# Kernel tuning notes

Measured on AMD Instinct MI355X. Metric: run time of the kernel, lower is better.

## Reference

```python
import jax, jax.numpy as jnp
import numpy as np

B, T, D, H = 8, 2048, 1024, 128  # batch, seq, input_size, head_size


def setup_inputs() -> dict:
    key = jax.random.key(0)
    kx, kq, kk, kv = jax.random.split(key, 4)
    s = 1.0 / np.sqrt(D)
    return {
        "x": jax.random.normal(kx, (B, T, D), dtype=jnp.float32),
        "Wq": jax.random.normal(kq, (D, H), dtype=jnp.float32) * s,
        "Wk": jax.random.normal(kk, (D, H), dtype=jnp.float32) * s,
        "Wv": jax.random.normal(kv, (D, H), dtype=jnp.float32) * s,
    }


def reference(x, Wq, Wk, Wv):
    # projections (Linear, no bias)
    q = jnp.einsum("btd,dh->bth", x, Wq)
    k = jnp.einsum("btd,dh->bth", x, Wk)
    v = jnp.einsum("btd,dh->bth", x, Wv)
    scale = H ** (-0.5)
    scores = jnp.einsum("bth,bsh->bts", q, k) * scale  # [B,T,T]
    t = x.shape[1]
    causal = jnp.tril(jnp.ones((t, t), dtype=bool))
    scores = jnp.where(causal, scores, -jnp.inf)
    attn = jax.nn.softmax(scores, axis=-1)  # dropout p=0.0 -> identity
    out = jnp.einsum("bts,bsh->bth", attn, v)
    return out
```

## Files before the change

### kernel.cpp

```cpp
#include <hip/hip_runtime.h>
#include <math.h>

#define B_ 8
#define T_ 2048
#define D_ 1024
#define H_ 128
#define BT (B_ * T_)

typedef short bf16x8 __attribute__((ext_vector_type(8)));
typedef short bf16x4 __attribute__((ext_vector_type(4)));
typedef float f32x4 __attribute__((ext_vector_type(4)));
typedef int i32x2 __attribute__((ext_vector_type(2)));

static constexpr float SCALE = 0.08838834764831845f;

__device__ inline unsigned short f2b(float f) {
  unsigned int u = __float_as_uint(f);
  u += 0x7FFF + ((u >> 16) & 1);
  return (unsigned short)(u >> 16);
}
__device__ inline unsigned int pk2(float a, float b) {
  return (unsigned int)f2b(a) | ((unsigned int)f2b(b) << 16);
}
__device__ __forceinline__ unsigned int pk2f(float a, float b) {
  unsigned int r;
  asm("v_cvt_pk_bf16_f32 %0, %1, %2" : "=v"(r) : "v"(a), "v"(b));
  return r;
}
__device__ __forceinline__ void mfma16(f32x4& d, bf16x4 a, bf16x4 b) {
  asm("v_mfma_f32_16x16x16_bf16 %0, %1, %2, %0" : "+v"(d) : "v"(a), "v"(b));
}

__device__ __forceinline__ void gll16(const void* g, void* l) {
  __builtin_amdgcn_global_load_lds(
      (const __attribute__((address_space(1))) void*)g,
      (__attribute__((address_space(3))) void*)l, 16, 0, 0);
}

__global__ __launch_bounds__(256) void wcvt_kernel(
    const float* __restrict__ Wq, const float* __restrict__ Wk,
    const float* __restrict__ Wv, short* __restrict__ Wt) {
  __shared__ short Wls[128 * 72];
  const int sel = blockIdx.y;
  const float* W = sel == 0 ? Wq : (sel == 1 ? Wk : Wv);
  const int d0 = blockIdx.x * 64;
  const int tid = threadIdx.x;
#pragma unroll
  for (int i = 0; i < 8; ++i) {
    int slot = tid + i * 256;
    int r = slot >> 5, hg = slot & 31;
    float4 w = *(const float4*)(W + (size_t)(d0 + r) * H_ + hg * 4);
    Wls[(hg * 4 + 0) * 72 + r] = (short)f2b(w.x);
    Wls[(hg * 4 + 1) * 72 + r] = (short)f2b(w.y);
    Wls[(hg * 4 + 2) * 72 + r] = (short)f2b(w.z);
    Wls[(hg * 4 + 3) * 72 + r] = (short)f2b(w.w);
  }
  __syncthreads();
  short* dst = Wt + (size_t)sel * D_ * H_;
#pragma unroll
  for (int i = 0; i < 4; ++i) {
    int slot = tid + i * 256;
    int h = slot >> 3, g = slot & 7;
    *(int4*)(dst + (size_t)h * D_ + d0 + g * 8) = *(int4*)&Wls[h * 72 + g * 8];
  }
}

__global__ __launch_bounds__(256) void proj_kernel(
    const float* __restrict__ x, const short* __restrict__ Wt,
    short* __restrict__ qb, short* __restrict__ kb, short* __restrict__ vtb) {
  __shared__ alignas(16) char smem[49152];
  short* Xs0 = (short*)smem;
  short* Xs1 = (short*)(smem + 8192);
  short* Ws0 = (short*)(smem + 16384);
  short* Ws1 = (short*)(smem + 32768);

  const int tid = threadIdx.x;
  const int wave = tid >> 6, lane = tid & 63;
  const int ln = lane & 15, quad = lane >> 4;
  const int mw = wave & 1, nw = wave >> 1;
  const int sel = blockIdx.y;
  const int row0 = blockIdx.x * 64;
  const short* W = Wt + (size_t)sel * (size_t)(D_ * H_);

  f32x4 acc[2][4];
#pragma unroll
  for (int mi = 0; mi < 2; ++mi)
#pragma unroll
    for (int ni = 0; ni < 4; ++ni) acc[mi][ni] = (f32x4){0.f, 0.f, 0.f, 0.f};

  auto stage = [&](int bf, int k0) {
    short* Ws = bf ? Ws1 : Ws0;
#pragma unroll
    for (int j = 0; j < 4; ++j) {
      const int rbase = wave * 32 + j * 8;
      const int n = rbase + (lane >> 3);
      const int gp = (lane & 7) ^ (n & 7);
      gll16(W + (size_t)n * D_ + k0 + gp * 8, (char*)Ws + rbase * 128);
    }
    short* Xs = bf ? Xs1 : Xs0;
    float4 xr[4];
#pragma unroll
    for (int i = 0; i < 4; ++i) {
      int fid = tid + i * 256;
      int r = fid >> 4, g4 = fid & 15;
      xr[i] = *(const float4*)(x + (size_t)(row0 + r) * D_ + k0 + g4 * 4);
    }
#pragma unroll
    for (int i = 0; i < 4; ++i) {
      int fid = tid + i * 256;
      int r = fid >> 4, g4 = fid & 15;
      int g = g4 >> 1, half = g4 & 1;
      unsigned int* p = (unsigned int*)&Xs[r * 64 + ((g ^ (r & 7)) * 8) + half * 4];
      p[0] = pk2f(xr[i].x, xr[i].y);
      p[1] = pk2f(xr[i].z, xr[i].w);
    }
  };

  stage(0, 0);
  for (int s = 0; s < 16; ++s) {
    __syncthreads();
    if (s < 15) stage((s + 1) & 1, (s + 1) * 64);
    const short* Xs = (s & 1) ? Xs1 : Xs0;
    const short* Ws = (s & 1) ? Ws1 : Ws0;
#pragma unroll
    for (int kk = 0; kk < 2; ++kk) {
      bf16x8 a[2];
#pragma unroll
      for (int mi = 0; mi < 2; ++mi) {
        int r = mw * 32 + mi * 16 + ln;
        a[mi] = *(bf16x8*)&Xs[r * 64 + (((kk * 4 + quad) ^ (r & 7)) * 8)];
      }
#pragma unroll
      for (int ni = 0; ni < 4; ++ni) {
        int n = nw * 64 + ni * 16 + ln;
        bf16x8 bb = *(bf16x8*)&Ws[n * 64 + (((kk * 4 + quad) ^ (n & 7)) * 8)];
#pragma unroll
        for (int mi = 0; mi < 2; ++mi)
          acc[mi][ni] = __builtin_amdgcn_mfma_f32_16x16x32_bf16(a[mi], bb, acc[mi][ni], 0, 0, 0);
      }
    }
  }

  __syncthreads();
  short* Cs = (short*)smem;
  if (sel < 2) {
    short* out = sel ? kb : qb;
#pragma unroll
    for (int mi = 0; mi < 2; ++mi)
#pragma unroll
      for (int ni = 0; ni < 4; ++ni)
#pragma unroll
        for (int rr = 0; rr < 4; ++rr)
          Cs[(mw * 32 + mi * 16 + quad * 4 + rr) * 136 + nw * 64 + ni * 16 + ln] =
              (short)f2b(acc[mi][ni][rr]);
    __syncthreads();
#pragma unroll
    for (int i = 0; i < 4; ++i) {
      int slot = tid + i * 256;
      int r = slot >> 4, g = slot & 15;
      *(int4*)(out + (size_t)(row0 + r) * H_ + g * 8) = *(int4*)&Cs[r * 136 + g * 8];
    }
  } else {
#pragma unroll
    for (int mi = 0; mi < 2; ++mi)
#pragma unroll
      for (int ni = 0; ni < 4; ++ni)
#pragma unroll
        for (int rr = 0; rr < 4; ++rr)
          Cs[(nw * 64 + ni * 16 + ln) * 72 + mw * 32 + mi * 16 + quad * 4 + rr] =
              (short)f2b(acc[mi][ni][rr]);
    __syncthreads();
    const int b = row0 >> 11, t0 = row0 & 2047;
#pragma unroll
    for (int i = 0; i < 4; ++i) {
      int slot = tid + i * 256;
      int h = slot >> 3, g = slot & 7;
      *(int4*)(vtb + (size_t)(b * H_ + h) * T_ + t0 + g * 8) = *(int4*)&Cs[h * 72 + g * 8];
    }
  }
}

__global__ __launch_bounds__(256, 5) void attn_part(
    const short* __restrict__ qb, const short* __restrict__ kb,
    const short* __restrict__ vtb, float* __restrict__ po,
    float* __restrict__ pm, float* __restrict__ pl,
    float* __restrict__ out) {
  __shared__ alignas(16) char smem[32768];
  short* Ks0 = (short*)smem;
  short* Ks1 = (short*)(smem + 8192);
  short* Vt0 = (short*)(smem + 16384);
  short* Vt1 = (short*)(smem + 24576);

  const int tid = threadIdx.x;
  const int wv = tid >> 6, lane = tid & 63;
  const int ln = lane & 15, quad = lane >> 4;
  const int b = blockIdx.x & 7;
  const int rr = 79 - (blockIdx.x >> 3);
  const int g = (rr >= 48) ? 3 : (rr >= 24) ? 2 : (rr >= 8) ? 1 : 0;
  const int local = rr - 4 * g * (g + 1);
  const int j = 8 * g + local / (g + 1);
  const int s = local - (local / (g + 1)) * (g + 1);
  const int nseg = g + 1;
  const int sid = b * 80 + rr;
  const int q0 = j * 64;
  const int nchunks = min(16, 2 * (j + 1) - 16 * s);

  const int qglob = q0 + wv * 16 + ln;

  bf16x8 qfr[4];
#pragma unroll
  for (int kk = 0; kk < 4; ++kk)
    qfr[kk] = *(const bf16x8*)(qb + (size_t)(b * T_ + q0 + wv * 16 + ln) * H_ +
                               kk * 32 + quad * 8);

  f32x4 oacc[8];
#pragma unroll
  for (int ht = 0; ht < 8; ++ht) oacc[ht] = (f32x4){0.f, 0.f, 0.f, 0.f};

  float m_run = -INFINITY, l_run = 0.f;

  auto stageK = [&](short* dst, int s0) {
#pragma unroll
    for (int jj = 0; jj < 2; ++jj) {
      const int rb = wv * 8 + jj * 4;
      const int r = rb + (lane >> 4);
      const int gp = (lane & 15) ^ (r & 7);
      gll16(kb + (size_t)(b * T_ + s0 + r) * H_ + gp * 8, (char*)dst + rb * 256);
    }
  };
  auto stageV = [&](short* dst, int s0) {
#pragma unroll
    for (int jj = 0; jj < 2; ++jj) {
      const int hb = wv * 32 + jj * 16;
      const int h = hb + (lane >> 2);
      const int gp = (lane & 3) ^ (h & 3) ^ ((h >> 2) & 3);
      gll16(vtb + (size_t)(b * H_ + h) * T_ + s0 + gp * 8, (char*)dst + hb * 64);
    }
  };

  stageK(Ks0, 512 * s);
  stageV(Vt0, 512 * s);

  for (int ch = 0; ch < nchunks; ++ch) {
    const int s0 = 512 * s + ch * 32;
    const int cur = ch & 1;
    __syncthreads();
    if (ch + 1 < nchunks) {
      stageK(cur ? Ks0 : Ks1, s0 + 32);
      stageV(cur ? Vt0 : Vt1, s0 + 32);
    }
    const short* Kc = cur ? Ks1 : Ks0;
    const short* Vc = cur ? Vt1 : Vt0;

    f32x4 sacc[2];
#pragma unroll
    for (int t = 0; t < 2; ++t) sacc[t] = (f32x4){0.f, 0.f, 0.f, 0.f};
#pragma unroll
    for (int kk = 0; kk < 4; ++kk) {
#pragma unroll
      for (int t = 0; t < 2; ++t) {
        const int krow = t * 16 + ln;
        bf16x8 kf = *(bf16x8*)&Kc[krow * 128 + (((kk * 4 + quad) ^ (krow & 7)) * 8)];
        sacc[t] = __builtin_amdgcn_mfma_f32_16x16x32_bf16(kf, qfr[kk], sacc[t], 0, 0, 0);
      }
    }

    float sv[2][4];
    float mc = -INFINITY;
    if (s0 + 31 <= q0 + wv * 16) {
#pragma unroll
      for (int t = 0; t < 2; ++t)
#pragma unroll
        for (int r = 0; r < 4; ++r) {
          sv[t][r] = sacc[t][r] * SCALE;
          mc = fmaxf(mc, sv[t][r]);
        }
    } else {
#pragma unroll
      for (int t = 0; t < 2; ++t)
#pragma unroll
        for (int r = 0; r < 4; ++r) {
          const int key = s0 + t * 16 + quad * 4 + r;
          float sc = sacc[t][r] * SCALE;
          sv[t][r] = (key <= qglob) ? sc : -INFINITY;
          mc = fmaxf(mc, sv[t][r]);
        }
    }
    mc = fmaxf(mc, __shfl_xor(mc, 16));
    mc = fmaxf(mc, __shfl_xor(mc, 32));

    if (!__all(mc <= m_run + 8.f)) {
      const float mnew = fmaxf(m_run, mc);
      const float alpha = __expf(m_run - mnew);
#pragma unroll
      for (int ht = 0; ht < 8; ++ht)
#pragma unroll
        for (int r = 0; r < 4; ++r) oacc[ht][r] *= alpha;
      l_run *= alpha;
      m_run = mnew;
    }
    float lc = 0.f;
    float p[2][4];
#pragma unroll
    for (int t = 0; t < 2; ++t)
#pragma unroll
      for (int r = 0; r < 4; ++r) {
        p[t][r] = __expf(sv[t][r] - m_run);
        lc += p[t][r];
      }
    lc += __shfl_xor(lc, 16);
    lc += __shfl_xor(lc, 32);
    l_run += lc;

#pragma unroll
    for (int t = 0; t < 2; ++t) {
      i32x2 pp = {(int)pk2f(p[t][0], p[t][1]), (int)pk2f(p[t][2], p[t][3])};
      bf16x4 pf = __builtin_bit_cast(bf16x4, pp);
      const int gsl = t * 2 + (quad >> 1);
      const int off = (quad & 1) * 4;
#pragma unroll
      for (int ht = 0; ht < 8; ++ht) {
        const int hrow = ht * 16 + ln;
        const int slot = gsl ^ ((hrow & 3) ^ ((hrow >> 2) & 3));
        bf16x4 vf = *(const bf16x4*)&Vc[hrow * 32 + slot * 8 + off];
        mfma16(oacc[ht], vf, pf);
      }
    }
  }

  float* Ot = (float*)smem;
  const int row = wv * 16 + ln;

  if (nseg == 1) {
    const float inv = 1.0f / l_run;
#pragma unroll
    for (int ht = 0; ht < 8; ++ht)
#pragma unroll
      for (int r = 0; r < 4; ++r) oacc[ht][r] *= inv;
    __syncthreads();
#pragma unroll
    for (int ht = 0; ht < 8; ++ht) {
      const int cg = (ht * 4 + quad) ^ (row & 31);
      *(f32x4*)&Ot[row * 128 + cg * 4] = oacc[ht];
    }
    __syncthreads();
    float* dst = out + (size_t)(b * T_ + q0) * H_;
#pragma unroll
    for (int i = 0; i < 8; ++i) {
      int slot2 = tid + i * 256;
      int r2 = slot2 >> 5, c2 = slot2 & 31;
      *(f32x4*)(dst + r2 * 128 + c2 * 4) =
          *(f32x4*)&Ot[r2 * 128 + ((c2 ^ (r2 & 31)) * 4)];
    }
    return;
  }

  if (quad == 0) {
    pm[(size_t)sid * 64 + wv * 16 + ln] = m_run;
    pl[(size_t)sid * 64 + wv * 16 + ln] = l_run;
  }
  __syncthreads();
#pragma unroll
  for (int ht = 0; ht < 8; ++ht) {
    const int cg = (ht * 4 + quad) ^ (row & 31);
    *(f32x4*)&Ot[row * 128 + cg * 4] = oacc[ht];
  }
  __syncthreads();
  float* dst = po + (size_t)sid * 8192;
#pragma unroll
  for (int i = 0; i < 8; ++i) {
    int slot2 = tid + i * 256;
    int r2 = slot2 >> 5, c2 = slot2 & 31;
    *(f32x4*)(dst + r2 * 128 + c2 * 4) =
        *(f32x4*)&Ot[r2 * 128 + ((c2 ^ (r2 & 31)) * 4)];
  }
}

__global__ __launch_bounds__(256) void attn_reduce(
    const float* __restrict__ po, const float* __restrict__ pm,
    const float* __restrict__ pl, float* __restrict__ out) {
  const int b = blockIdx.x / 24;
  const int j = 8 + (blockIdx.x % 24);
  const int g = j >> 3;
  const int nseg = g + 1;
  const int sid0 = b * 80 + 4 * g * (g + 1) + (j - 8 * g) * nseg;
  const int tid = threadIdx.x;
  const int q = tid >> 2, hq = tid & 3;

  float m[4], l[4], a[4];
  float M = -INFINITY;
  for (int s2 = 0; s2 < nseg; ++s2) {
    m[s2] = pm[(size_t)(sid0 + s2) * 64 + q];
    l[s2] = pl[(size_t)(sid0 + s2) * 64 + q];
    M = fmaxf(M, m[s2]);
  }
  float lsum = 0.f;
  for (int s2 = 0; s2 < nseg; ++s2) {
    a[s2] = __expf(m[s2] - M);
    lsum += a[s2] * l[s2];
  }
  f32x4 acc[8];
#pragma unroll
  for (int i = 0; i < 8; ++i) acc[i] = (f32x4){0.f, 0.f, 0.f, 0.f};
  for (int s2 = 0; s2 < nseg; ++s2) {
    const float* src = po + (size_t)(sid0 + s2) * 8192 + q * 128 + hq * 32;
    const float as = a[s2];
#pragma unroll
    for (int i = 0; i < 8; ++i) {
      f32x4 v = *(const f32x4*)(src + i * 4);
#pragma unroll
      for (int c = 0; c < 4; ++c) acc[i][c] += as * v[c];
    }
  }
  const float inv = 1.0f / lsum;
  float* o = out + ((size_t)(b * T_ + j * 64 + q)) * H_ + hq * 32;
#pragma unroll
  for (int i = 0; i < 8; ++i) {
    f32x4 v;
#pragma unroll
    for (int c = 0; c < 4; ++c) v[c] = acc[i][c] * inv;
    *(f32x4*)(o + i * 4) = v;
  }
}

extern "C" void kernel_launch(void* const* d_in, const int* in_sizes, int n_in,
                              void* d_out, int out_size, void* d_ws, size_t ws_size,
                              hipStream_t stream) {
  const float* x  = (const float*)d_in[0];
  const float* Wq = (const float*)d_in[1];
  const float* Wk = (const float*)d_in[2];
  const float* Wv = (const float*)d_in[3];
  float* out = (float*)d_out;

  char* ws = (char*)d_ws;
  short* qb  = (short*)(ws);
  short* kb  = (short*)(ws + 4194304);
  short* vtb = (short*)(ws + 8388608);
  short* Wt  = (short*)(ws + 12582912);
  float* po  = (float*)(ws + 14680064);
  float* pm  = (float*)(ws + 35651584);
  float* pl  = (float*)(ws + 35815424);

  wcvt_kernel<<<dim3(D_ / 64, 3), 256, 0, stream>>>(Wq, Wk, Wv, Wt);
  proj_kernel<<<dim3(BT / 64, 3), 256, 0, stream>>>(x, Wt, qb, kb, vtb);
  attn_part<<<dim3(8 * 80), 256, 0, stream>>>(qb, kb, vtb, po, pm, pl, out);
  attn_reduce<<<dim3(8 * 24), 256, 0, stream>>>(po, pm, pl, out);
}
```

Before: 155.0 us.

## Double attention query tile to 128 rows with 512-thread blocks sharing K/V stages

The attention-partial kernel now processes 128 query rows per block using 8 waves (512 threads) instead of 64 rows with 4 waves. Each staged 32-key K/V chunk in LDS is therefore reused by twice as many query rows, halving global K/V traffic and halving the block count. The split-K segmentation, partial-buffer indexing and the reduce kernel are adjusted to match. The output epilogue is written in two 64-row halves through the same LDS buffer. In exchange there are fewer blocks (320) to fill the GPU, coarser causal-diagonal work imbalance, and larger blocks whose occupancy must still fit the register budget.

```diff
diff --git a/kernel.cpp b/kernel.cpp
--- a/kernel.cpp
+++ b/kernel.cpp
@@ -180,7 +180,7 @@
   }
 }
 
-__global__ __launch_bounds__(256, 5) void attn_part(
+__global__ __launch_bounds__(512, 4) void attn_part(
     const short* __restrict__ qb, const short* __restrict__ kb,
     const short* __restrict__ vtb, float* __restrict__ po,
     float* __restrict__ pm, float* __restrict__ pl,
@@ -195,15 +195,15 @@
   const int wv = tid >> 6, lane = tid & 63;
   const int ln = lane & 15, quad = lane >> 4;
   const int b = blockIdx.x & 7;
-  const int rr = 79 - (blockIdx.x >> 3);
-  const int g = (rr >= 48) ? 3 : (rr >= 24) ? 2 : (rr >= 8) ? 1 : 0;
-  const int local = rr - 4 * g * (g + 1);
-  const int j = 8 * g + local / (g + 1);
-  const int s = local - (local / (g + 1)) * (g + 1);
+  const int rr = 39 - (blockIdx.x >> 3);
+  const int g = (rr >= 24) ? 3 : (rr >= 12) ? 2 : (rr >= 4) ? 1 : 0;
   const int nseg = g + 1;
-  const int sid = b * 80 + rr;
-  const int q0 = j * 64;
-  const int nchunks = min(16, 2 * (j + 1) - 16 * s);
+  const int local = rr - 2 * g * (g + 1);
+  const int j2 = 4 * g + local / nseg;
+  const int s = local - (local / nseg) * nseg;
+  const int sid = b * 40 + rr;
+  const int q0 = j2 * 128;
+  const int nchunks = min(16, 4 * (j2 + 1) - 16 * s);
 
   const int qglob = q0 + wv * 16 + ln;
 
@@ -220,22 +220,16 @@
   float m_run = -INFINITY, l_run = 0.f;
 
   auto stageK = [&](short* dst, int s0) {
-#pragma unroll
-    for (int jj = 0; jj < 2; ++jj) {
-      const int rb = wv * 8 + jj * 4;
-      const int r = rb + (lane >> 4);
-      const int gp = (lane & 15) ^ (r & 7);
-      gll16(kb + (size_t)(b * T_ + s0 + r) * H_ + gp * 8, (char*)dst + rb * 256);
-    }
+    const int rb = wv * 4;
+    const int r = rb + (lane >> 4);
+    const int gp = (lane & 15) ^ (r & 7);
+    gll16(kb + (size_t)(b * T_ + s0 + r) * H_ + gp * 8, (char*)dst + rb * 256);
   };
   auto stageV = [&](short* dst, int s0) {
-#pragma unroll
-    for (int jj = 0; jj < 2; ++jj) {
-      const int hb = wv * 32 + jj * 16;
-      const int h = hb + (lane >> 2);
-      const int gp = (lane & 3) ^ (h & 3) ^ ((h >> 2) & 3);
-      gll16(vtb + (size_t)(b * H_ + h) * T_ + s0 + gp * 8, (char*)dst + hb * 64);
-    }
+    const int hb = wv * 16;
+    const int h = hb + (lane >> 2);
+    const int gp = (lane & 3) ^ (h & 3) ^ ((h >> 2) & 3);
+    gll16(vtb + (size_t)(b * H_ + h) * T_ + s0 + gp * 8, (char*)dst + hb * 64);
   };
 
   stageK(Ks0, 512 * s);
@@ -329,7 +323,8 @@
   }
 
   float* Ot = (float*)smem;
-  const int row = wv * 16 + ln;
+  const int hw = wv >> 2;
+  const int lr = (wv & 3) * 16 + ln;
 
   if (nseg == 1) {
     const float inv = 1.0f / l_run;
@@ -337,42 +332,52 @@
     for (int ht = 0; ht < 8; ++ht)
 #pragma unroll
       for (int r = 0; r < 4; ++r) oacc[ht][r] *= inv;
-    __syncthreads();
-#pragma unroll
-    for (int ht = 0; ht < 8; ++ht) {
-      const int cg = (ht * 4 + quad) ^ (row & 31);
-      *(f32x4*)&Ot[row * 128 + cg * 4] = oacc[ht];
-    }
-    __syncthreads();
-    float* dst = out + (size_t)(b * T_ + q0) * H_;
-#pragma unroll
-    for (int i = 0; i < 8; ++i) {
-      int slot2 = tid + i * 256;
+#pragma unroll
+    for (int half = 0; half < 2; ++half) {
+      __syncthreads();
+      if (hw == half) {
+#pragma unroll
+        for (int ht = 0; ht < 8; ++ht) {
+          const int cg = (ht * 4 + quad) ^ (lr & 31);
+          *(f32x4*)&Ot[lr * 128 + cg * 4] = oacc[ht];
+        }
+      }
+      __syncthreads();
+      float* dst = out + (size_t)(b * T_ + q0 + half * 64) * H_;
+#pragma unroll
+      for (int i = 0; i < 4; ++i) {
+        int slot2 = tid + i * 512;
+        int r2 = slot2 >> 5, c2 = slot2 & 31;
+        *(f32x4*)(dst + r2 * 128 + c2 * 4) =
+            *(f32x4*)&Ot[r2 * 128 + ((c2 ^ (r2 & 31)) * 4)];
+      }
+    }
+    return;
+  }
+
+  if (quad == 0) {
+    pm[(size_t)sid * 128 + wv * 16 + ln] = m_run;
+    pl[(size_t)sid * 128 + wv * 16 + ln] = l_run;
+  }
+#pragma unroll
+  for (int half = 0; half < 2; ++half) {
+    __syncthreads();
+    if (hw == half) {
+#pragma unroll
+      for (int ht = 0; ht < 8; ++ht) {
+        const int cg = (ht * 4 + quad) ^ (lr & 31);
+        *(f32x4*)&Ot[lr * 128 + cg * 4] = oacc[ht];
+      }
+    }
+    __syncthreads();
+    float* dst = po + (size_t)sid * 16384 + half * 8192;
+#pragma unroll
+    for (int i = 0; i < 4; ++i) {
+      int slot2 = tid + i * 512;
       int r2 = slot2 >> 5, c2 = slot2 & 31;
       *(f32x4*)(dst + r2 * 128 + c2 * 4) =
           *(f32x4*)&Ot[r2 * 128 + ((c2 ^ (r2 & 31)) * 4)];
     }
-    return;
-  }
-
-  if (quad == 0) {
-    pm[(size_t)sid * 64 + wv * 16 + ln] = m_run;
-    pl[(size_t)sid * 64 + wv * 16 + ln] = l_run;
-  }
-  __syncthreads();
-#pragma unroll
-  for (int ht = 0; ht < 8; ++ht) {
-    const int cg = (ht * 4 + quad) ^ (row & 31);
-    *(f32x4*)&Ot[row * 128 + cg * 4] = oacc[ht];
-  }
-  __syncthreads();
-  float* dst = po + (size_t)sid * 8192;
-#pragma unroll
-  for (int i = 0; i < 8; ++i) {
-    int slot2 = tid + i * 256;
-    int r2 = slot2 >> 5, c2 = slot2 & 31;
-    *(f32x4*)(dst + r2 * 128 + c2 * 4) =
-        *(f32x4*)&Ot[r2 * 128 + ((c2 ^ (r2 & 31)) * 4)];
   }
 }
 
@@ -381,17 +386,20 @@
     const float* __restrict__ pl, float* __restrict__ out) {
   const int b = blockIdx.x / 24;
   const int j = 8 + (blockIdx.x % 24);
-  const int g = j >> 3;
+  const int j2 = j >> 1;
+  const int half = j & 1;
+  const int g = j2 >> 2;
   const int nseg = g + 1;
-  const int sid0 = b * 80 + 4 * g * (g + 1) + (j - 8 * g) * nseg;
+  const int sid0 = b * 40 + 2 * g * (g + 1) + (j2 - 4 * g) * nseg;
   const int tid = threadIdx.x;
   const int q = tid >> 2, hq = tid & 3;
+  const int row = half * 64 + q;
 
   float m[4], l[4], a[4];
   float M = -INFINITY;
   for (int s2 = 0; s2 < nseg; ++s2) {
-    m[s2] = pm[(size_t)(sid0 + s2) * 64 + q];
-    l[s2] = pl[(size_t)(sid0 + s2) * 64 + q];
+    m[s2] = pm[(size_t)(sid0 + s2) * 128 + row];
+    l[s2] = pl[(size_t)(sid0 + s2) * 128 + row];
     M = fmaxf(M, m[s2]);
   }
   float lsum = 0.f;
@@ -403,7 +411,7 @@
 #pragma unroll
   for (int i = 0; i < 8; ++i) acc[i] = (f32x4){0.f, 0.f, 0.f, 0.f};
   for (int s2 = 0; s2 < nseg; ++s2) {
-    const float* src = po + (size_t)(sid0 + s2) * 8192 + q * 128 + hq * 32;
+    const float* src = po + (size_t)(sid0 + s2) * 16384 + row * 128 + hq * 32;
     const float as = a[s2];
 #pragma unroll
     for (int i = 0; i < 8; ++i) {
@@ -443,6 +451,6 @@
 
   wcvt_kernel<<<dim3(D_ / 64, 3), 256, 0, stream>>>(Wq, Wk, Wv, Wt);
   proj_kernel<<<dim3(BT / 64, 3), 256, 0, stream>>>(x, Wt, qb, kb, vtb);
-  attn_part<<<dim3(8 * 80), 256, 0, stream>>>(qb, kb, vtb, po, pm, pl, out);
+  attn_part<<<dim3(8 * 40), 512, 0, stream>>>(qb, kb, vtb, po, pm, pl, out);
   attn_reduce<<<dim3(8 * 24), 256, 0, stream>>>(po, pm, pl, out);
 }
```

Result: slower. 159.1 us (+2.7%).
